# Kernel optimization log

Measured on AMD Instinct MI355X. Metric: run time of the kernel, lower is better.

Reference implementation:

```python
import jax, jax.numpy as jnp
import numpy as np

B, T, D, H, S = 512, 256, 128, 128, 32


def _param(key, shape, scale):
    return (jax.random.normal(key, shape, dtype=jnp.float32) * scale)


def setup_inputs() -> dict:
    key = jax.random.key(0)
    ks = jax.random.split(key, 32)
    sD = 1.0 / np.sqrt(D)
    sH = 1.0 / np.sqrt(H)
    inp = {
        'x': jax.random.normal(ks[0], (B, T, D), dtype=jnp.float32),
        'statics': jax.random.normal(ks[1], (B, S), dtype=jnp.float32),
        'mask': (jax.random.uniform(ks[2], (B, T, D)) > 0.5).astype(jnp.float32),
        'delta': jax.random.uniform(ks[3], (B, T, D), dtype=jnp.float32),
        'x_last_observed': jax.random.normal(ks[4], (B, T, D), dtype=jnp.float32),
        'x_mean': jax.random.normal(ks[5], (B, D), dtype=jnp.float32),
        'hs0': jax.random.normal(ks[6], (B, H), dtype=jnp.float32),
        # GRU-D decay params
        'w_dg_x': _param(ks[7], (D,), sD), 'b_dg_x': jnp.zeros((D,), jnp.float32),
        'W_dg_h': _param(ks[8], (H, D), sD), 'b_dg_h': jnp.zeros((H,), jnp.float32),
        # gates: update z, reset r, candidate h
        'W_z': _param(ks[9], (H, D), sD), 'U_z': _param(ks[10], (H, H), sH),
        'V_z': _param(ks[11], (H, D), sD), 'b_z': jnp.zeros((H,), jnp.float32),
        'W_r': _param(ks[12], (H, D), sD), 'U_r': _param(ks[13], (H, H), sH),
        'V_r': _param(ks[14], (H, D), sD), 'b_r': jnp.zeros((H,), jnp.float32),
        'W_h': _param(ks[15], (H, D), sD), 'U_h': _param(ks[16], (H, H), sH),
        'V_h': _param(ks[17], (H, D), sD), 'b_h': jnp.zeros((H,), jnp.float32),
        # classifier
        'W_out': _param(ks[18], (1, H + S), 1.0 / np.sqrt(H + S)),
        'b_out': jnp.zeros((1,), jnp.float32),
    }
    return inp


def reference(x, statics, mask, delta, x_last_observed, x_mean, hs0,
              w_dg_x, b_dg_x, W_dg_h, b_dg_h,
              W_z, U_z, V_z, b_z, W_r, U_r, V_r, b_r,
              W_h, U_h, V_h, b_h, W_out, b_out):
    # scan over time: inputs [T, B, D]
    xs = jnp.transpose(x, (1, 0, 2))
    ms = jnp.transpose(mask, (1, 0, 2))
    ds = jnp.transpose(delta, (1, 0, 2))
    xl = jnp.transpose(x_last_observed, (1, 0, 2))

    def step(h, inputs):
        xv, m, d, xlast = inputs
        gamma_x = jnp.exp(-jax.nn.relu(w_dg_x * d + b_dg_x))            # [B, D]
        gamma_h = jnp.exp(-jax.nn.relu(d @ W_dg_h.T + b_dg_h))          # [B, H]
        x_hat = m * xv + (1.0 - m) * (gamma_x * xlast + (1.0 - gamma_x) * x_mean)
        h = gamma_h * h
        z = jax.nn.sigmoid(x_hat @ W_z.T + h @ U_z.T + m @ V_z.T + b_z)
        r = jax.nn.sigmoid(x_hat @ W_r.T + h @ U_r.T + m @ V_r.T + b_r)
        h_tilde = jnp.tanh(x_hat @ W_h.T + (r * h) @ U_h.T + m @ V_h.T + b_h)
        h = (1.0 - z) * h + z * h_tilde
        return h, None

    h_final, _ = jax.lax.scan(step, hs0, (xs, ms, ds, xl))
    full = jnp.concatenate([h_final, statics], axis=1)                  # [B, H+S]
    predictions = full @ W_out.T + b_out                                # [B, 1]
    return predictions
```

## Files before the change

kernel.cpp:

```cpp
#include <hip/hip_runtime.h>
#include <stdint.h>


#define B_ 512
#define T_ 256
#define D_ 128
#define H_ 128
#define S_ 32
#define NE 512
#define KA 384
#define M_ (B_*T_)
#define HP 136
#define ESLAB ((size_t)NE * 16)
#define ESTRIDE ((size_t)32 * ESLAB)

typedef __attribute__((ext_vector_type(8))) short short8;
typedef __attribute__((ext_vector_type(4))) float f32x4;

__device__ __forceinline__ unsigned short f2bf(float f) {
  union { float f; uint32_t u; } v; v.f = f;
  return (unsigned short)((v.u + 0x7FFFu + ((v.u >> 16) & 1u)) >> 16);
}
__device__ __forceinline__ float bf2f(uint32_t s) {
  union { uint32_t u; float f; } v; v.u = s << 16;
  return v.f;
}

__device__ __forceinline__ uint2  ldraw(const unsigned short* p) { return *(const uint2*)p; }
__device__ __forceinline__ float4 ldraw(const float* p)          { return *(const float4*)p; }
__device__ __forceinline__ void unp(uint2 v, float o[4]) {
  o[0] = bf2f(v.x & 0xffffu); o[1] = bf2f(v.x >> 16);
  o[2] = bf2f(v.y & 0xffffu); o[3] = bf2f(v.y >> 16);
}
__device__ __forceinline__ void unp(float4 v, float o[4]) {
  o[0] = v.x; o[1] = v.y; o[2] = v.z; o[3] = v.w;
}
__device__ __forceinline__ void st4(unsigned short* p, const float v[4]) {
  uint2 u;
  u.x = (uint32_t)f2bf(v[0]) | ((uint32_t)f2bf(v[1]) << 16);
  u.y = (uint32_t)f2bf(v[2]) | ((uint32_t)f2bf(v[3]) << 16);
  *(uint2*)p = u;
}
__device__ __forceinline__ void st4(float* p, const float v[4]) {
  *(float4*)p = make_float4(v[0], v[1], v[2], v[3]);
}

__device__ __forceinline__ float fsigmoid(float x) {
  return __builtin_amdgcn_rcpf(1.f + __expf(-x));
}
__device__ __forceinline__ float ftanh(float x) {
  return 1.f - 2.f * __builtin_amdgcn_rcpf(1.f + __expf(2.f * x));
}

#define ASYNC_CP16(gsrc, ldst) \
  __builtin_amdgcn_global_load_lds((const __attribute__((address_space(1))) void*)(gsrc), \
                                   (__attribute__((address_space(3))) void*)(ldst), 16, 0, 0)

__global__ void prep_weights(const float* __restrict__ Wz, const float* __restrict__ Vz,
                             const float* __restrict__ Wr, const float* __restrict__ Vr,
                             const float* __restrict__ Wh, const float* __restrict__ Vh,
                             const float* __restrict__ Wdgh,
                             const float* __restrict__ bz, const float* __restrict__ br,
                             const float* __restrict__ bh, const float* __restrict__ bdgh,
                             unsigned short* __restrict__ Wcat, float* __restrict__ bias)
{
  int id = blockIdx.x * 256 + threadIdx.x;
  if (id < NE * KA) {
    int n = id / KA, k = id - n * KA;
    float v = 0.f;
    if (n < 384) {
      int nn = n & 127;
      const float* W = (n < 128) ? Wz : (n < 256) ? Wr : Wh;
      const float* V = (n < 128) ? Vz : (n < 256) ? Vr : Vh;
      if (k < 128)      v = W[nn * 128 + k];
      else if (k < 256) v = V[nn * 128 + (k - 128)];
    } else {
      if (k >= 256) v = Wdgh[(n - 384) * 128 + (k - 256)];
    }
    Wcat[id] = f2bf(v);
  }
  if (id < NE) {
    bias[id] = (id < 128) ? bz[id] : (id < 256) ? br[id - 128]
             : (id < 384) ? bh[id - 256] : bdgh[id - 384];
  }
}

__global__ void build_A(const float* __restrict__ x, const float* __restrict__ mask,
                        const float* __restrict__ delta, const float* __restrict__ xlast,
                        const float* __restrict__ xmean,
                        const float* __restrict__ wdgx, const float* __restrict__ bdgx,
                        unsigned short* __restrict__ Abuf)
{
  int id = blockIdx.x * 256 + threadIdx.x;
  int m = id >> 5;
  int c = id & 31;
  int t = m >> 9;
  int b = m & (B_ - 1);
  int k = c * 4;
  size_t src = ((size_t)b * T_ + t) * D_ + k;
  float4 xv = *(const float4*)(x + src);
  float4 mv = *(const float4*)(mask + src);
  float4 dv = *(const float4*)(delta + src);
  float4 lv = *(const float4*)(xlast + src);
  float4 uv = *(const float4*)(xmean + (size_t)b * D_ + k);
  float4 wv = *(const float4*)(wdgx + k);
  float4 bv = *(const float4*)(bdgx + k);
  const float* xp = (const float*)&xv; const float* mp = (const float*)&mv;
  const float* dp = (const float*)&dv; const float* lp = (const float*)&lv;
  const float* up = (const float*)&uv; const float* wp = (const float*)&wv;
  const float* bp = (const float*)&bv;
  unsigned short xh[4], mm[4], dd[4];
  #pragma unroll
  for (int i = 0; i < 4; ++i) {
    float g = __expf(-fmaxf(wp[i] * dp[i] + bp[i], 0.f));
    float xhat = mp[i] * xp[i] + (1.f - mp[i]) * (g * lp[i] + (1.f - g) * up[i]);
    xh[i] = f2bf(xhat); mm[i] = f2bf(mp[i]); dd[i] = f2bf(dp[i]);
  }
  uint2 px, pm, pd;
  px.x = (uint32_t)xh[0] | ((uint32_t)xh[1] << 16); px.y = (uint32_t)xh[2] | ((uint32_t)xh[3] << 16);
  pm.x = (uint32_t)mm[0] | ((uint32_t)mm[1] << 16); pm.y = (uint32_t)mm[2] | ((uint32_t)mm[3] << 16);
  pd.x = (uint32_t)dd[0] | ((uint32_t)dd[1] << 16); pd.y = (uint32_t)dd[2] | ((uint32_t)dd[3] << 16);
  unsigned short* rowp = Abuf + (size_t)m * KA;
  *(uint2*)(rowp + k)       = px;
  *(uint2*)(rowp + 128 + k) = pm;
  *(uint2*)(rowp + 256 + k) = pd;
}

template <typename ET>
__global__ __launch_bounds__(256, 2) void gemm_phase1(
    const unsigned short* __restrict__ Abuf, const unsigned short* __restrict__ Wcat,
    const float* __restrict__ bias, ET* __restrict__ E)
{
  __shared__ unsigned short As[128 * 32];
  __shared__ unsigned short Bs[128 * 32];
  const int tid = threadIdx.x;
  const int wave = tid >> 6, lane = tid & 63;
  const int q = lane >> 4, rl = lane & 15;
  const int m0 = blockIdx.x * 128;
  const int n0 = blockIdx.y * 128;
  const int wm = (wave >> 1) * 64, wn = (wave & 1) * 64;

  f32x4 acc[4][4];
  #pragma unroll
  for (int a = 0; a < 4; ++a)
    #pragma unroll
    for (int b = 0; b < 4; ++b) acc[a][b] = (f32x4){0.f, 0.f, 0.f, 0.f};

  for (int kt = 0; kt < KA / 32; ++kt) {
    const int kbase = kt * 32;
    #pragma unroll
    for (int i = 0; i < 2; ++i) {
      int chunk = i * 256 + wave * 64 + lane;
      int row = chunk >> 2, kc = chunk & 3;
      ASYNC_CP16(Abuf + (size_t)(m0 + row) * KA + kbase + kc * 8,
                 As + (size_t)(i * 256 + wave * 64) * 8);
      ASYNC_CP16(Wcat + (size_t)(n0 + row) * KA + kbase + kc * 8,
                 Bs + (size_t)(i * 256 + wave * 64) * 8);
    }
    __syncthreads();
    short8 af[4], bfr[4];
    #pragma unroll
    for (int tm = 0; tm < 4; ++tm)
      af[tm] = *(const short8*)(As + (wm + tm * 16 + rl) * 32 + q * 8);
    #pragma unroll
    for (int tn = 0; tn < 4; ++tn)
      bfr[tn] = *(const short8*)(Bs + (wn + tn * 16 + rl) * 32 + q * 8);
    #pragma unroll
    for (int tm = 0; tm < 4; ++tm)
      #pragma unroll
      for (int tn = 0; tn < 4; ++tn)
        acc[tm][tn] = __builtin_amdgcn_mfma_f32_16x16x32_bf16(af[tm], bfr[tn], acc[tm][tn], 0, 0, 0);
    __syncthreads();
  }

  const int t = m0 >> 9;
  const int bbase = m0 & (B_ - 1);
  #pragma unroll
  for (int tn = 0; tn < 4; ++tn) {
    int n = n0 + wn + tn * 16 + rl;
    float bv = bias[n];
    bool isg = (n >= 384);
    #pragma unroll
    for (int tm = 0; tm < 4; ++tm) {
      int brow = bbase + wm + tm * 16;
      float v[4];
      #pragma unroll
      for (int reg = 0; reg < 4; ++reg) {
        float xv = acc[tm][tn][reg] + bv;
        v[reg] = isg ? __expf(-fmaxf(xv, 0.f)) : xv;
      }
      st4(E + ((size_t)t * 32 + (brow >> 4)) * ESLAB + (size_t)n * 16 + q * 4, v);
    }
  }
}

template <typename ET>
__global__ __launch_bounds__(512, 2) void grud_scan(
    const ET* __restrict__ E,
    const float* __restrict__ Uz, const float* __restrict__ Ur, const float* __restrict__ Uh,
    const float* __restrict__ hs0, const float* __restrict__ statics,
    const float* __restrict__ Wout, const float* __restrict__ bout,
    float* __restrict__ out)
{
  __shared__ unsigned short hdec[16 * HP];
  __shared__ unsigned short rhb[16 * HP];
  __shared__ float hfin[16 * HP];
  const int tid = threadIdx.x;
  const int wave = tid >> 6, lane = tid & 63;
  const int q = lane >> 4, rl = lane & 15;
  const int col = wave * 16 + rl;
  const int b0 = blockIdx.x * 16;

  short8 uz[4], ur[4], uh[4];
  #pragma unroll
  for (int kc = 0; kc < 4; ++kc) {
    int koff = kc * 32 + q * 8;
    const float* pzw = Uz + col * H_ + koff;
    const float* prw = Ur + col * H_ + koff;
    const float* phw = Uh + col * H_ + koff;
    #pragma unroll
    for (int j = 0; j < 8; ++j) {
      uz[kc][j] = (short)f2bf(pzw[j]);
      ur[kc][j] = (short)f2bf(prw[j]);
      uh[kc][j] = (short)f2bf(phw[j]);
    }
  }

  const ET* pz = E + (size_t)blockIdx.x * ESLAB + (size_t)col * 16 + q * 4;
  const ET* pr = pz + 128 * 16;
  const ET* ph = pz + 256 * 16;
  const ET* pg = pz + 384 * 16;

  using RawT = decltype(ldraw((const ET*)nullptr));
  RawT cz, cr, chh, cg, nz{}, nr{}, nh{}, ng{};
  cz  = ldraw(pz);
  cr  = ldraw(pr);
  chh = ldraw(ph);
  cg  = ldraw(pg + ESTRIDE);
  RawT g0raw = ldraw(pg);

  float hd[4], g0[4];
  unp(g0raw, g0);
  #pragma unroll
  for (int reg = 0; reg < 4; ++reg) {
    int row = q * 4 + reg;
    float h0 = hs0[(b0 + row) * H_ + col];
    hd[reg] = g0[reg] * h0;
    hdec[row * HP + col] = f2bf(hd[reg]);
  }
  __syncthreads();

  for (int t = 0; t < T_; ++t) {
    if (t + 1 < T_) {
      size_t off = (size_t)(t + 1) * ESTRIDE;
      nz = ldraw(pz + off); nr = ldraw(pr + off); nh = ldraw(ph + off);
      if (t + 2 < T_) ng = ldraw(pg + (size_t)(t + 2) * ESTRIDE);
    }
    float Pz[4], Pr[4], Ph[4];
    unp(cz, Pz); unp(cr, Pr); unp(chh, Ph);

    short8 af[4];
    #pragma unroll
    for (int kc = 0; kc < 4; ++kc)
      af[kc] = *(const short8*)(&hdec[rl * HP + kc * 32 + q * 8]);
    f32x4 accz = (f32x4){0.f,0.f,0.f,0.f}, accr = (f32x4){0.f,0.f,0.f,0.f};
    #pragma unroll
    for (int kc = 0; kc < 4; ++kc) {
      accz = __builtin_amdgcn_mfma_f32_16x16x32_bf16(af[kc], uz[kc], accz, 0, 0, 0);
      accr = __builtin_amdgcn_mfma_f32_16x16x32_bf16(af[kc], ur[kc], accr, 0, 0, 0);
    }
    float zz[4];
    #pragma unroll
    for (int reg = 0; reg < 4; ++reg) {
      zz[reg] = fsigmoid(accz[reg] + Pz[reg]);
      float rr = fsigmoid(accr[reg] + Pr[reg]);
      rhb[(q * 4 + reg) * HP + col] = f2bf(rr * hd[reg]);
    }
    __syncthreads();

    short8 ar[4];
    #pragma unroll
    for (int kc = 0; kc < 4; ++kc)
      ar[kc] = *(const short8*)(&rhb[rl * HP + kc * 32 + q * 8]);
    f32x4 acch = (f32x4){0.f,0.f,0.f,0.f};
    #pragma unroll
    for (int kc = 0; kc < 4; ++kc)
      acch = __builtin_amdgcn_mfma_f32_16x16x32_bf16(ar[kc], uh[kc], acch, 0, 0, 0);

    if (t < T_ - 1) {
      float Gn[4];
      unp(cg, Gn);
      #pragma unroll
      for (int reg = 0; reg < 4; ++reg) {
        float ht = ftanh(acch[reg] + Ph[reg]);
        float hn = hd[reg] + zz[reg] * (ht - hd[reg]);
        hd[reg] = Gn[reg] * hn;
        hdec[(q * 4 + reg) * HP + col] = f2bf(hd[reg]);
      }
    } else {
      #pragma unroll
      for (int reg = 0; reg < 4; ++reg) {
        float ht = ftanh(acch[reg] + Ph[reg]);
        float hn = hd[reg] + zz[reg] * (ht - hd[reg]);
        hfin[(q * 4 + reg) * HP + col] = hn;
      }
    }
    __syncthreads();

    cz = nz; cr = nr; chh = nh; cg = ng;
  }

  {
    int row = tid >> 5, j = tid & 31;
    float acc = 0.f;
    #pragma unroll
    for (int c0 = 0; c0 < 4; ++c0)
      acc += hfin[row * HP + j + c0 * 32] * Wout[j + c0 * 32];
    acc += statics[(size_t)(b0 + row) * S_ + j] * Wout[H_ + j];
    #pragma unroll
    for (int off = 16; off >= 1; off >>= 1)
      acc += __shfl_down(acc, off, 32);
    if (j == 0) out[b0 + row] = acc + bout[0];
  }
}

template <typename ET>
static void launch_all(void* const* d_in, float* out, char* ws, hipStream_t stream)
{
  const float* x      = (const float*)d_in[0];
  const float* statics= (const float*)d_in[1];
  const float* mask   = (const float*)d_in[2];
  const float* delta  = (const float*)d_in[3];
  const float* xlast  = (const float*)d_in[4];
  const float* xmean  = (const float*)d_in[5];
  const float* hs0    = (const float*)d_in[6];
  const float* wdgx   = (const float*)d_in[7];
  const float* bdgx   = (const float*)d_in[8];
  const float* Wdgh   = (const float*)d_in[9];
  const float* bdgh   = (const float*)d_in[10];
  const float* Wz     = (const float*)d_in[11];
  const float* Uz     = (const float*)d_in[12];
  const float* Vz     = (const float*)d_in[13];
  const float* bz     = (const float*)d_in[14];
  const float* Wr     = (const float*)d_in[15];
  const float* Ur     = (const float*)d_in[16];
  const float* Vr     = (const float*)d_in[17];
  const float* br     = (const float*)d_in[18];
  const float* Wh     = (const float*)d_in[19];
  const float* Uh     = (const float*)d_in[20];
  const float* Vh     = (const float*)d_in[21];
  const float* bh     = (const float*)d_in[22];
  const float* Wout   = (const float*)d_in[23];
  const float* bout   = (const float*)d_in[24];

  const size_t eBytes = (size_t)M_ * NE * sizeof(ET);
  const size_t aBytes = (size_t)M_ * KA * 2;
  const size_t wBytes = (size_t)NE * KA * 2;
  ET* E = (ET*)ws;
  unsigned short* Abuf = (unsigned short*)(ws + eBytes);
  unsigned short* Wcat = (unsigned short*)(ws + eBytes + aBytes);
  float* bias = (float*)(ws + eBytes + aBytes + wBytes);

  prep_weights<<<768, 256, 0, stream>>>(Wz, Vz, Wr, Vr, Wh, Vh, Wdgh,
                                        bz, br, bh, bdgh, Wcat, bias);
  build_A<<<(M_ * 32) / 256, 256, 0, stream>>>(x, mask, delta, xlast, xmean,
                                               wdgx, bdgx, Abuf);
  gemm_phase1<ET><<<dim3(M_ / 128, NE / 128), 256, 0, stream>>>(Abuf, Wcat, bias, E);
  grud_scan<ET><<<B_ / 16, 512, 0, stream>>>(E, Uz, Ur, Uh, hs0, statics, Wout, bout, out);
}

extern "C" void kernel_launch(void* const* d_in, const int* in_sizes, int n_in,
                              void* d_out, int out_size, void* d_ws, size_t ws_size,
                              hipStream_t stream)
{
  char* ws = (char*)d_ws;
  float* out = (float*)d_out;
  const size_t common = (size_t)M_ * KA * 2 + (size_t)NE * KA * 2 + 4096;
  const size_t needF32 = (size_t)M_ * NE * 4 + common;
  const size_t needBF  = (size_t)M_ * NE * 2 + common;
  if (ws_size >= needF32)     launch_all<float>(d_in, out, ws, stream);
  else if (ws_size >= needBF) launch_all<unsigned short>(d_in, out, ws, stream);
}
```

Measured before the change: 602.0 us.

## Fuse GEMM and scan into one persistent kernel with per-timestep flags

```diff
diff --git a/kernel.cpp b/kernel.cpp
--- a/kernel.cpp
+++ b/kernel.cpp
@@ -11,6 +11,7 @@
 #define KA 384
 #define M_ (B_*T_)
 #define HP 136
+#define NSCAN 32
 #define ESLAB ((size_t)NE * 16)
 #define ESTRIDE ((size_t)32 * ESLAB)
 
@@ -20,6 +21,10 @@
 __device__ __forceinline__ unsigned short f2bf(float f) {
   union { float f; uint32_t u; } v; v.f = f;
   return (unsigned short)((v.u + 0x7FFFu + ((v.u >> 16) & 1u)) >> 16);
+}
+__device__ __forceinline__ unsigned short f2bf_fast(float f) {
+  union { float f; uint32_t u; } v; v.f = f;
+  return (unsigned short)((v.u + 0x8000u) >> 16);
 }
 __device__ __forceinline__ float bf2f(uint32_t s) {
   union { uint32_t u; float f; } v; v.u = s << 16;
@@ -127,62 +132,56 @@
 }
 
 template <typename ET>
-__global__ __launch_bounds__(256, 2) void gemm_phase1(
+__device__ __forceinline__ void gemm_body(
+    int g, char* smem,
     const unsigned short* __restrict__ Abuf, const unsigned short* __restrict__ Wcat,
-    const float* __restrict__ bias, ET* __restrict__ E)
-{
-  __shared__ unsigned short As[128 * 32];
-  __shared__ unsigned short Bs[128 * 32];
+    const float* __restrict__ bias, ET* __restrict__ E, int* __restrict__ sync)
+{
   const int tid = threadIdx.x;
   const int wave = tid >> 6, lane = tid & 63;
   const int q = lane >> 4, rl = lane & 15;
-  const int m0 = blockIdx.x * 128;
-  const int n0 = blockIdx.y * 128;
-  const int wm = (wave >> 1) * 64, wn = (wave & 1) * 64;
-
-  f32x4 acc[4][4];
+  const int t = g >> 4, sub = g & 15, mi = sub >> 2, ni = sub & 3;
+  const int bbase = mi * 128, n0 = ni * 128;
+  const size_t arow0 = (size_t)t * B_ + bbase;
+  unsigned short* As = (unsigned short*)smem;
+  unsigned short* Bs = As + 4096;
+  const int wr = (wave >> 2) * 64, wc = (wave & 3) * 32;
+  const int srow = tid >> 2, skc = tid & 3;
+
+  f32x4 acc[4][2];
   #pragma unroll
   for (int a = 0; a < 4; ++a)
     #pragma unroll
-    for (int b = 0; b < 4; ++b) acc[a][b] = (f32x4){0.f, 0.f, 0.f, 0.f};
+    for (int b = 0; b < 2; ++b) acc[a][b] = (f32x4){0.f, 0.f, 0.f, 0.f};
 
   for (int kt = 0; kt < KA / 32; ++kt) {
     const int kbase = kt * 32;
-    #pragma unroll
-    for (int i = 0; i < 2; ++i) {
-      int chunk = i * 256 + wave * 64 + lane;
-      int row = chunk >> 2, kc = chunk & 3;
-      ASYNC_CP16(Abuf + (size_t)(m0 + row) * KA + kbase + kc * 8,
-                 As + (size_t)(i * 256 + wave * 64) * 8);
-      ASYNC_CP16(Wcat + (size_t)(n0 + row) * KA + kbase + kc * 8,
-                 Bs + (size_t)(i * 256 + wave * 64) * 8);
-    }
+    ASYNC_CP16(Abuf + (arow0 + srow) * KA + kbase + skc * 8, As + (size_t)tid * 8);
+    ASYNC_CP16(Wcat + (size_t)(n0 + srow) * KA + kbase + skc * 8, Bs + (size_t)tid * 8);
     __syncthreads();
-    short8 af[4], bfr[4];
+    short8 af[4], bfr[2];
     #pragma unroll
     for (int tm = 0; tm < 4; ++tm)
-      af[tm] = *(const short8*)(As + (wm + tm * 16 + rl) * 32 + q * 8);
-    #pragma unroll
-    for (int tn = 0; tn < 4; ++tn)
-      bfr[tn] = *(const short8*)(Bs + (wn + tn * 16 + rl) * 32 + q * 8);
+      af[tm] = *(const short8*)(As + (wr + tm * 16 + rl) * 32 + q * 8);
+    #pragma unroll
+    for (int tn = 0; tn < 2; ++tn)
+      bfr[tn] = *(const short8*)(Bs + (wc + tn * 16 + rl) * 32 + q * 8);
     #pragma unroll
     for (int tm = 0; tm < 4; ++tm)
       #pragma unroll
-      for (int tn = 0; tn < 4; ++tn)
+      for (int tn = 0; tn < 2; ++tn)
         acc[tm][tn] = __builtin_amdgcn_mfma_f32_16x16x32_bf16(af[tm], bfr[tn], acc[tm][tn], 0, 0, 0);
     __syncthreads();
   }
 
-  const int t = m0 >> 9;
-  const int bbase = m0 & (B_ - 1);
   #pragma unroll
-  for (int tn = 0; tn < 4; ++tn) {
-    int n = n0 + wn + tn * 16 + rl;
+  for (int tn = 0; tn < 2; ++tn) {
+    int n = n0 + wc + tn * 16 + rl;
     float bv = bias[n];
     bool isg = (n >= 384);
     #pragma unroll
     for (int tm = 0; tm < 4; ++tm) {
-      int brow = bbase + wm + tm * 16;
+      int brow = bbase + wr + tm * 16;
       float v[4];
       #pragma unroll
       for (int reg = 0; reg < 4; ++reg) {
@@ -192,19 +191,37 @@
       st4(E + ((size_t)t * 32 + (brow >> 4)) * ESLAB + (size_t)n * 16 + q * 4, v);
     }
   }
+  __syncthreads();
+  if (tid == 0) {
+    int old = __hip_atomic_fetch_add(&sync[t], 1, __ATOMIC_ACQ_REL, __HIP_MEMORY_SCOPE_AGENT);
+    if (old == 15) {
+      int* wmp = sync + T_;
+      while (__hip_atomic_load(wmp, __ATOMIC_ACQUIRE, __HIP_MEMORY_SCOPE_AGENT) < t)
+        __builtin_amdgcn_s_sleep(4);
+      __hip_atomic_store(wmp, t + 1, __ATOMIC_RELEASE, __HIP_MEMORY_SCOPE_AGENT);
+    }
+  }
 }
 
 template <typename ET>
-__global__ __launch_bounds__(512, 2) void grud_scan(
-    const ET* __restrict__ E,
+__global__ __launch_bounds__(512, 2) void fused_gemm_scan(
+    const unsigned short* __restrict__ Abuf, const unsigned short* __restrict__ Wcat,
+    const float* __restrict__ bias, ET* __restrict__ E, int* __restrict__ sync,
     const float* __restrict__ Uz, const float* __restrict__ Ur, const float* __restrict__ Uh,
     const float* __restrict__ hs0, const float* __restrict__ statics,
     const float* __restrict__ Wout, const float* __restrict__ bout,
     float* __restrict__ out)
 {
-  __shared__ unsigned short hdec[16 * HP];
-  __shared__ unsigned short rhb[16 * HP];
-  __shared__ float hfin[16 * HP];
+  __shared__ __align__(16) char smem[17408];
+  if (blockIdx.x >= NSCAN) {
+    gemm_body<ET>(blockIdx.x - NSCAN, smem, Abuf, Wcat, bias, E, sync);
+    return;
+  }
+
+  unsigned short* hdec = (unsigned short*)smem;
+  unsigned short* rhb  = hdec + 16 * HP;
+  float* hfin = (float*)(smem + 4 * 16 * HP);
+  int* wmp = sync + T_;
   const int tid = threadIdx.x;
   const int wave = tid >> 6, lane = tid & 63;
   const int q = lane >> 4, rl = lane & 15;
@@ -231,6 +248,12 @@
   const ET* ph = pz + 256 * 16;
   const ET* pg = pz + 384 * 16;
 
+  int cw = __hip_atomic_load(wmp, __ATOMIC_ACQUIRE, __HIP_MEMORY_SCOPE_AGENT);
+  while (cw < 2) {
+    __builtin_amdgcn_s_sleep(8);
+    cw = __hip_atomic_load(wmp, __ATOMIC_ACQUIRE, __HIP_MEMORY_SCOPE_AGENT);
+  }
+
   using RawT = decltype(ldraw((const ET*)nullptr));
   RawT cz, cr, chh, cg, nz{}, nr{}, nh{}, ng{};
   cz  = ldraw(pz);
@@ -246,12 +269,17 @@
     int row = q * 4 + reg;
     float h0 = hs0[(b0 + row) * H_ + col];
     hd[reg] = g0[reg] * h0;
-    hdec[row * HP + col] = f2bf(hd[reg]);
+    hdec[row * HP + col] = f2bf_fast(hd[reg]);
   }
   __syncthreads();
 
   for (int t = 0; t < T_; ++t) {
     if (t + 1 < T_) {
+      const int need = (t + 2 < T_) ? (t + 3) : (t + 2);
+      while (cw < need) {
+        cw = __hip_atomic_load(wmp, __ATOMIC_ACQUIRE, __HIP_MEMORY_SCOPE_AGENT);
+        if (cw < need) __builtin_amdgcn_s_sleep(8);
+      }
       size_t off = (size_t)(t + 1) * ESTRIDE;
       nz = ldraw(pz + off); nr = ldraw(pr + off); nh = ldraw(ph + off);
       if (t + 2 < T_) ng = ldraw(pg + (size_t)(t + 2) * ESTRIDE);
@@ -274,7 +302,7 @@
     for (int reg = 0; reg < 4; ++reg) {
       zz[reg] = fsigmoid(accz[reg] + Pz[reg]);
       float rr = fsigmoid(accr[reg] + Pr[reg]);
-      rhb[(q * 4 + reg) * HP + col] = f2bf(rr * hd[reg]);
+      rhb[(q * 4 + reg) * HP + col] = f2bf_fast(rr * hd[reg]);
     }
     __syncthreads();
 
@@ -295,7 +323,7 @@
         float ht = ftanh(acch[reg] + Ph[reg]);
         float hn = hd[reg] + zz[reg] * (ht - hd[reg]);
         hd[reg] = Gn[reg] * hn;
-        hdec[(q * 4 + reg) * HP + col] = f2bf(hd[reg]);
+        hdec[(q * 4 + reg) * HP + col] = f2bf_fast(hd[reg]);
       }
     } else {
       #pragma unroll
@@ -360,13 +388,15 @@
   unsigned short* Abuf = (unsigned short*)(ws + eBytes);
   unsigned short* Wcat = (unsigned short*)(ws + eBytes + aBytes);
   float* bias = (float*)(ws + eBytes + aBytes + wBytes);
+  int* sync = (int*)(ws + eBytes + aBytes + wBytes + 2048);
 
   prep_weights<<<768, 256, 0, stream>>>(Wz, Vz, Wr, Vr, Wh, Vh, Wdgh,
                                         bz, br, bh, bdgh, Wcat, bias);
   build_A<<<(M_ * 32) / 256, 256, 0, stream>>>(x, mask, delta, xlast, xmean,
                                                wdgx, bdgx, Abuf);
-  gemm_phase1<ET><<<dim3(M_ / 128, NE / 128), 256, 0, stream>>>(Abuf, Wcat, bias, E);
-  grud_scan<ET><<<B_ / 16, 512, 0, stream>>>(E, Uz, Ur, Uh, hs0, statics, Wout, bout, out);
+  hipMemsetAsync(sync, 0, (T_ + 1) * sizeof(int), stream);
+  fused_gemm_scan<ET><<<NSCAN + 16 * T_, 512, 0, stream>>>(
+      Abuf, Wcat, bias, E, sync, Uz, Ur, Uh, hs0, statics, Wout, bout, out);
 }
 
 extern "C" void kernel_launch(void* const* d_in, const int* in_sizes, int n_in,
@@ -375,7 +405,7 @@
 {
   char* ws = (char*)d_ws;
   float* out = (float*)d_out;
-  const size_t common = (size_t)M_ * KA * 2 + (size_t)NE * KA * 2 + 4096;
+  const size_t common = (size_t)M_ * KA * 2 + (size_t)NE * KA * 2 + 8192;
   const size_t needF32 = (size_t)M_ * NE * 4 + common;
   const size_t needBF  = (size_t)M_ * NE * 2 + common;
   if (ws_size >= needF32)     launch_all<float>(d_in, out, ws, stream);
```

New measurement: 1.988 ms. 3.3x slower.
